# Kernel optimization log

Measured on AMD Instinct MI355X. Metric: run time of the kernel, lower is better.

The kernel has to match this reference:

```python
import jax, jax.numpy as jnp
import numpy as np

DIM = 2048
N_HEADS = 16
N_KV_HEADS = 4
HEAD_DIM = DIM // N_HEADS  # 128
N_REP = N_HEADS // N_KV_HEADS
MAX_SEQ_LEN = 4096
SEQLEN = 4096


def setup_inputs() -> dict:
    key = jax.random.key(0)
    ks = jax.random.split(key, 6)
    x = jax.random.normal(ks[0], (1, SEQLEN, DIM), dtype=jnp.float32)
    # rotary frequencies, llama-style theta=10000
    inv_freq = 1.0 / (10000.0 ** (np.arange(0, HEAD_DIM, 2, dtype=np.float32) / HEAD_DIM))
    t = np.arange(SEQLEN, dtype=np.float32)
    ang = np.outer(t, inv_freq)  # [S, head_dim/2]
    freqs_cos = jnp.asarray(np.cos(ang))
    freqs_sin = jnp.asarray(np.sin(ang))
    # additive causal mask [S, S]
    mask = jnp.where(jnp.tril(jnp.ones((SEQLEN, SEQLEN), dtype=bool)), 0.0, -1e9).astype(jnp.float32)
    sc = 0.02
    wq = jax.random.normal(ks[1], (DIM, N_HEADS * HEAD_DIM), dtype=jnp.float32) * sc
    wk = jax.random.normal(ks[2], (DIM, N_KV_HEADS * HEAD_DIM), dtype=jnp.float32) * sc
    wv = jax.random.normal(ks[3], (DIM, N_KV_HEADS * HEAD_DIM), dtype=jnp.float32) * sc
    wo = jax.random.normal(ks[4], (N_HEADS * HEAD_DIM, DIM), dtype=jnp.float32) * sc
    return {"x": x, "start_pos": 0, "freqs_cos": freqs_cos, "freqs_sin": freqs_sin,
            "mask": mask, "wq": wq, "wk": wk, "wv": wv, "wo": wo}


def _rope(x, cos, sin):
    # x: [b, s, h, d]; cos/sin: [s, d/2]; consecutive pairs form complex numbers
    b, s, h, d = x.shape
    xr = x.astype(jnp.float32).reshape(b, s, h, d // 2, 2)
    x1, x2 = xr[..., 0], xr[..., 1]
    c = cos[None, :, None, :]
    sn = sin[None, :, None, :]
    o1 = x1 * c - x2 * sn
    o2 = x1 * sn + x2 * c
    return jnp.stack([o1, o2], axis=-1).reshape(b, s, h, d).astype(x.dtype)


def reference(x, start_pos, freqs_cos, freqs_sin, mask, wq, wk, wv, wo):
    bsz, seqlen, _ = x.shape
    xq = (x @ wq).reshape(bsz, seqlen, N_HEADS, HEAD_DIM)
    xk = (x @ wk).reshape(bsz, seqlen, N_KV_HEADS, HEAD_DIM)
    xv = (x @ wv).reshape(bsz, seqlen, N_KV_HEADS, HEAD_DIM)
    xq = _rope(xq, freqs_cos, freqs_sin)
    xk = _rope(xk, freqs_cos, freqs_sin)
    # KV-cache append (cache is zeros before this call)
    cache_k = jnp.zeros((1, MAX_SEQ_LEN, N_KV_HEADS, HEAD_DIM), dtype=xk.dtype)
    cache_v = jnp.zeros((1, MAX_SEQ_LEN, N_KV_HEADS, HEAD_DIM), dtype=xv.dtype)
    cache_k = jax.lax.dynamic_update_slice(cache_k, xk, (0, start_pos, 0, 0))
    cache_v = jax.lax.dynamic_update_slice(cache_v, xv, (0, start_pos, 0, 0))
    keys = cache_k[:bsz, : start_pos + seqlen]    # [b, T, kvh, d]
    values = cache_v[:bsz, : start_pos + seqlen]
    # GQA repeat to full head count
    keys = jnp.repeat(keys, N_REP, axis=2)
    values = jnp.repeat(values, N_REP, axis=2)
    scale = 1.0 / jnp.sqrt(jnp.float32(HEAD_DIM))
    scores = jnp.einsum('bshd,bthd->bhst', xq, keys) * scale  # [b, h, s, T]
    scores = scores + mask[None, None, :, :]
    probs = jax.nn.softmax(scores.astype(jnp.float32), axis=-1).astype(xq.dtype)
    out = jnp.einsum('bhst,bthd->bshd', probs, values).reshape(bsz, seqlen, -1)
    return out @ wo
```

## Files before the change

### kernel.cpp

```cpp
#include <hip/hip_runtime.h>
#include <hip/hip_bf16.h>
#include <stdint.h>

#define SEQ 4096
#define DIM 2048
#define NH 16
#define NKV 4
#define HD 128
#define KVLD 1024


using frag8 = __attribute__((ext_vector_type(8))) short;
using f32x4 = __attribute__((ext_vector_type(4))) float;

union VecU { ushort u[8]; uint4 v; };

__device__ __forceinline__ float bf2f(ushort u) {
    union { uint32_t u; float f; } v; v.u = ((uint32_t)u) << 16; return v.f;
}
__device__ __forceinline__ ushort f2bf(float f) {
    union { float f; uint32_t u; } v; v.f = f;
    uint32_t r = v.u + 0x7fffu + ((v.u >> 16) & 1u);
    return (ushort)(r >> 16);
}

__device__ __forceinline__ void glds16(const void* g, void* l) {
    __builtin_amdgcn_global_load_lds(
        (const __attribute__((address_space(1))) void*)g,
        (__attribute__((address_space(3))) void*)l, 16, 0, 0);
}

__global__ __launch_bounds__(256) void cvt_kernel(
    const float* __restrict__ src, ushort* __restrict__ dst)
{
    size_t i = ((size_t)blockIdx.x * 256 + threadIdx.x) * 8;
    float4 f0 = *(const float4*)&src[i];
    float4 f1 = *(const float4*)&src[i + 4];
    VecU t;
    t.u[0] = f2bf(f0.x); t.u[1] = f2bf(f0.y); t.u[2] = f2bf(f0.z); t.u[3] = f2bf(f0.w);
    t.u[4] = f2bf(f1.x); t.u[5] = f2bf(f1.y); t.u[6] = f2bf(f1.z); t.u[7] = f2bf(f1.w);
    *(uint4*)&dst[i] = t.v;
}

__global__ __launch_bounds__(256) void convW_kernel(
    const float* __restrict__ wq, const float* __restrict__ wk,
    const float* __restrict__ wv, ushort* __restrict__ WqT,
    ushort* __restrict__ KVT)
{
    __shared__ ushort T[32][36];
    const int K = DIM;
    const float* src; ushort* dst; int N, bn;
    int bx = blockIdx.x;
    if (bx < 64)      { src = wq; dst = WqT;                     N = DIM; bn = bx * 32; }
    else if (bx < 80) { src = wk; dst = KVT;                     N = 512; bn = (bx - 64) * 32; }
    else              { src = wv; dst = KVT + (size_t)512 * DIM; N = 512; bn = (bx - 80) * 32; }

    int r  = threadIdx.x >> 3;
    int c4 = (threadIdx.x & 7) * 4;
    int bk = blockIdx.y * 32;
    float4 v = *(const float4*)&src[(size_t)(bk + r) * N + bn + c4];
    T[r][c4]     = f2bf(v.x); T[r][c4 + 1] = f2bf(v.y);
    T[r][c4 + 2] = f2bf(v.z); T[r][c4 + 3] = f2bf(v.w);
    __syncthreads();
    ushort4 o;
    o.x = T[c4][r]; o.y = T[c4 + 1][r]; o.z = T[c4 + 2][r]; o.w = T[c4 + 3][r];
    *(ushort4*)&dst[(size_t)(bn + r) * K + bk + c4] = o;
}

__global__ __launch_bounds__(256) void convT_kernel(
    const float* __restrict__ src, ushort* __restrict__ dst, int K, int N)
{
    __shared__ ushort T[32][36];
    int r  = threadIdx.x >> 3;
    int c4 = (threadIdx.x & 7) * 4;
    int bk = blockIdx.y * 32, bn = blockIdx.x * 32;
    float4 v = *(const float4*)&src[(size_t)(bk + r) * N + bn + c4];
    T[r][c4]     = f2bf(v.x); T[r][c4 + 1] = f2bf(v.y);
    T[r][c4 + 2] = f2bf(v.z); T[r][c4 + 3] = f2bf(v.w);
    __syncthreads();
    ushort4 o;
    o.x = T[c4][r]; o.y = T[c4 + 1][r]; o.z = T[c4 + 2][r]; o.w = T[c4 + 3][r];
    *(ushort4*)&dst[(size_t)(bn + r) * K + bk + c4] = o;
}

__global__ __launch_bounds__(256) void fuse3_kernel(
    ushort* __restrict__ Qb, ushort* __restrict__ KVb, ushort* __restrict__ VT,
    const float* __restrict__ Cos, const float* __restrict__ Sin)
{
    __shared__ ushort T[32][36];
    int b = blockIdx.x;
    if (b < 20480) {
        ushort* X; int log2nh, strideT, idx; float osc;
        if (b < 16384) { X = Qb;  log2nh = 4; strideT = DIM;  osc = 0.08838834764831845f; idx = b * 256 + threadIdx.x; }
        else           { X = KVb; log2nh = 2; strideT = KVLD; osc = 1.0f; idx = (b - 16384) * 256 + threadIdx.x; }
        int p = idx & 63;
        int h = (idx >> 6) & ((1 << log2nh) - 1);
        int t = idx >> (6 + log2nh);
        size_t base = (size_t)t * strideT + (size_t)h * 128 + 2 * p;
        ushort2 xv = *(ushort2*)&X[base];
        float x1 = bf2f(xv.x), x2 = bf2f(xv.y);
        float c = Cos[t * 64 + p], s = Sin[t * 64 + p];
        ushort2 ov;
        ov.x = f2bf((x1 * c - x2 * s) * osc);
        ov.y = f2bf((x1 * s + x2 * c) * osc);
        *(ushort2*)&X[base] = ov;
    } else {
        int v  = b - 20480;
        int bd = (v & 15) * 32;
        int bt = (v >> 4) * 32;
        int r  = threadIdx.x >> 3;
        int c4 = (threadIdx.x & 7) * 4;
        ushort4 w = *(const ushort4*)&KVb[(size_t)(bt + r) * KVLD + 512 + bd + c4];
        T[r][c4] = w.x; T[r][c4 + 1] = w.y; T[r][c4 + 2] = w.z; T[r][c4 + 3] = w.w;
        __syncthreads();
        ushort4 o;
        o.x = T[c4][r]; o.y = T[c4 + 1][r]; o.z = T[c4 + 2][r]; o.w = T[c4 + 3][r];
        *(ushort4*)&VT[(size_t)(bd + r) * SEQ + bt + c4] = o;
    }
}

template <int CF>
__global__ __launch_bounds__(256) void gemm_tn(
    const ushort* __restrict__ A, const ushort* __restrict__ BT,
    void* __restrict__ C, int M, int N, int K)
{
    __shared__ ushort As[128 * 32];
    __shared__ ushort Bs[128 * 32];

    const int tid  = threadIdx.x;
    const int lane = tid & 63;
    const int wave = tid >> 6;
    const int bm   = blockIdx.y * 128;
    const int bn   = blockIdx.x * 128;
    const int wm   = (wave >> 1) * 64;
    const int wn   = (wave & 1) * 64;
    const int quad = lane >> 4;
    const int t16  = lane & 15;
    const int kg   = quad ^ ((t16 >> 1) & 3);

    f32x4 acc[4][4] = {};

    for (int k0 = 0; k0 < K; k0 += 32) {
        #pragma unroll
        for (int it = 0; it < 2; ++it) {
            int gid = it * 256 + tid;
            int r   = gid >> 2;
            int cs  = (gid & 3) ^ ((gid >> 3) & 3);
            glds16(&A[(size_t)(bm + r) * K + k0 + cs * 8],
                   &As[(it * 256 + wave * 64) * 8]);
            glds16(&BT[(size_t)(bn + r) * K + k0 + cs * 8],
                   &Bs[(it * 256 + wave * 64) * 8]);
        }
        __syncthreads();

        frag8 af[4], bf[4];
        #pragma unroll
        for (int i = 0; i < 4; ++i)
            af[i] = *(const frag8*)&As[(wm + i * 16 + t16) * 32 + kg * 8];
        #pragma unroll
        for (int j = 0; j < 4; ++j)
            bf[j] = *(const frag8*)&Bs[(wn + j * 16 + t16) * 32 + kg * 8];
        #pragma unroll
        for (int i = 0; i < 4; ++i)
            #pragma unroll
            for (int j = 0; j < 4; ++j)
                acc[i][j] = __builtin_amdgcn_mfma_f32_16x16x32_bf16(
                    af[i], bf[j], acc[i][j], 0, 0, 0);
        __syncthreads();
    }

    #pragma unroll
    for (int i = 0; i < 4; ++i)
        #pragma unroll
        for (int j = 0; j < 4; ++j)
            #pragma unroll
            for (int r = 0; r < 4; ++r) {
                int row = bm + wm + i * 16 + quad * 4 + r;
                int col = bn + wn + j * 16 + t16;
                if (CF) ((float*)C)[(size_t)row * N + col] = acc[i][j][r];
                else    ((ushort*)C)[(size_t)row * N + col] = f2bf(acc[i][j][r]);
            }
}

__global__ __launch_bounds__(256) void gemm_qkv(
    const ushort* __restrict__ A, const ushort* __restrict__ BT,
    ushort* __restrict__ Cq, ushort* __restrict__ Ckv)
{
    const int K = DIM;
    __shared__ ushort As[128 * 32];
    __shared__ ushort Bs[128 * 32];

    const int tid  = threadIdx.x;
    const int lane = tid & 63;
    const int wave = tid >> 6;
    const int bm   = blockIdx.y * 128;
    const int bn   = blockIdx.x * 128;
    const int wm   = (wave >> 1) * 64;
    const int wn   = (wave & 1) * 64;
    const int quad = lane >> 4;
    const int t16  = lane & 15;
    const int kg   = quad ^ ((t16 >> 1) & 3);

    f32x4 acc[4][4] = {};

    for (int k0 = 0; k0 < K; k0 += 32) {
        #pragma unroll
        for (int it = 0; it < 2; ++it) {
            int gid = it * 256 + tid;
            int r   = gid >> 2;
            int cs  = (gid & 3) ^ ((gid >> 3) & 3);
            glds16(&A[(size_t)(bm + r) * K + k0 + cs * 8],
                   &As[(it * 256 + wave * 64) * 8]);
            glds16(&BT[(size_t)(bn + r) * K + k0 + cs * 8],
                   &Bs[(it * 256 + wave * 64) * 8]);
        }
        __syncthreads();

        frag8 af[4], bf[4];
        #pragma unroll
        for (int i = 0; i < 4; ++i)
            af[i] = *(const frag8*)&As[(wm + i * 16 + t16) * 32 + kg * 8];
        #pragma unroll
        for (int j = 0; j < 4; ++j)
            bf[j] = *(const frag8*)&Bs[(wn + j * 16 + t16) * 32 + kg * 8];
        #pragma unroll
        for (int i = 0; i < 4; ++i)
            #pragma unroll
            for (int j = 0; j < 4; ++j)
                acc[i][j] = __builtin_amdgcn_mfma_f32_16x16x32_bf16(
                    af[i], bf[j], acc[i][j], 0, 0, 0);
        __syncthreads();
    }

    ushort* C;
    int ldc, cb;
    if (bn < 2048) { C = Cq;  ldc = DIM;  cb = 0; }
    else           { C = Ckv; ldc = KVLD; cb = 2048; }

    #pragma unroll
    for (int i = 0; i < 4; ++i)
        #pragma unroll
        for (int j = 0; j < 4; ++j)
            #pragma unroll
            for (int r = 0; r < 4; ++r) {
                int row = bm + wm + i * 16 + quad * 4 + r;
                int col = bn + wn + j * 16 + t16;
                C[(size_t)row * ldc + (col - cb)] = f2bf(acc[i][j][r]);
            }
}

__global__ __launch_bounds__(256, 2) void attn_kernel(
    const ushort* __restrict__ Q, const ushort* __restrict__ Kb,
    const ushort* __restrict__ VT, ushort* __restrict__ Oab,
    ushort* __restrict__ Oev, float2* __restrict__ lmE, float2* __restrict__ lmO)
{
    __shared__ ushort Ks[64][136];
    __shared__ ushort Vt[128][72];
    __shared__ ushort Sp[4][32][72];

    const int tid  = threadIdx.x;
    const int lane = tid & 63;
    const int wave = tid >> 6;
    const int quad = lane >> 4;
    const int t16  = lane & 15;
    const int hp   = blockIdx.x;
    const int hA   = 2 * hp;
    const int hB   = 2 * hp + 1;
    const int kvh  = hp >> 1;

    frag8 vONE;
    #pragma unroll
    for (int i = 0; i < 8; ++i) vONE[i] = (short)0x3F80;

    const int by = (int)blockIdx.y;
    int qt, c, split;
    if (by < 64) { split = 1; qt = 63 - (by >> 1); c = by & 1; }
    else         { split = 0; qt = 95 - by;        c = 0;      }
    const int n  = qt + 1;
    const int q0 = qt * 64;
    const int qwave = q0 + wave * 16;
    const int qmaxw = qwave + 15;
    const int tstart = (split && c) ? (n / 2) * 64 : 0;
    const int tend   = (split && !c) ? (n / 2) * 64 : n * 64;

    frag8 aQA[4], aQB[4];
    #pragma unroll
    for (int kk = 0; kk < 4; ++kk) {
        aQA[kk] = *(const frag8*)&Q[(size_t)(qwave + t16) * DIM + hA * HD + kk * 32 + quad * 8];
        aQB[kk] = *(const frag8*)&Q[(size_t)(qwave + t16) * DIM + hB * HD + kk * 32 + quad * 8];
    }

    f32x4 oA[8] = {}, oB[8] = {};
    f32x4 o9A = {0.f, 0.f, 0.f, 0.f};
    f32x4 o9B = {0.f, 0.f, 0.f, 0.f};
    float mA[4] = {0.f, 0.f, 0.f, 0.f};
    float mB[4] = {0.f, 0.f, 0.f, 0.f};

    for (int t0 = tstart; t0 < tend; t0 += 64) {
        #pragma unroll
        for (int it = 0; it < 4; ++it) {
            int idx = tid + it * 256;
            int tt  = idx >> 4;
            int cc  = (idx & 15) * 8;
            *(uint4*)&Ks[tt][cc] =
                *(const uint4*)&Kb[(size_t)(t0 + tt) * KVLD + kvh * HD + cc];
        }
        #pragma unroll
        for (int it = 0; it < 4; ++it) {
            int idx = tid + it * 256;
            int d   = idx >> 3;
            int tq  = (idx & 7) * 8;
            *(uint4*)&Vt[d][tq] =
                *(const uint4*)&VT[(size_t)(kvh * HD + d) * SEQ + t0 + tq];
        }
        __syncthreads();

        const bool hi = (t0 + 32 <= qmaxw);

        f32x4 sA0 = {0.f,0.f,0.f,0.f}, sA1 = {0.f,0.f,0.f,0.f};
        f32x4 sA2 = {0.f,0.f,0.f,0.f}, sA3 = {0.f,0.f,0.f,0.f};
        f32x4 sB0 = {0.f,0.f,0.f,0.f}, sB1 = {0.f,0.f,0.f,0.f};
        f32x4 sB2 = {0.f,0.f,0.f,0.f}, sB3 = {0.f,0.f,0.f,0.f};

        __builtin_amdgcn_s_setprio(1);
        #pragma unroll
        for (int kk = 0; kk < 4; ++kk) {
            frag8 b0 = *(const frag8*)&Ks[2 * t16][kk * 32 + quad * 8];
            frag8 b1 = *(const frag8*)&Ks[2 * t16 + 1][kk * 32 + quad * 8];
            sA0 = __builtin_amdgcn_mfma_f32_16x16x32_bf16(aQA[kk], b0, sA0, 0, 0, 0);
            sB0 = __builtin_amdgcn_mfma_f32_16x16x32_bf16(aQB[kk], b0, sB0, 0, 0, 0);
            sA1 = __builtin_amdgcn_mfma_f32_16x16x32_bf16(aQA[kk], b1, sA1, 0, 0, 0);
            sB1 = __builtin_amdgcn_mfma_f32_16x16x32_bf16(aQB[kk], b1, sB1, 0, 0, 0);
        }
        if (hi) {
            #pragma unroll
            for (int kk = 0; kk < 4; ++kk) {
                frag8 b2 = *(const frag8*)&Ks[32 + 2 * t16][kk * 32 + quad * 8];
                frag8 b3 = *(const frag8*)&Ks[33 + 2 * t16][kk * 32 + quad * 8];
                sA2 = __builtin_amdgcn_mfma_f32_16x16x32_bf16(aQA[kk], b2, sA2, 0, 0, 0);
                sB2 = __builtin_amdgcn_mfma_f32_16x16x32_bf16(aQB[kk], b2, sB2, 0, 0, 0);
                sA3 = __builtin_amdgcn_mfma_f32_16x16x32_bf16(aQA[kk], b3, sA3, 0, 0, 0);
                sB3 = __builtin_amdgcn_mfma_f32_16x16x32_bf16(aQB[kk], b3, sB3, 0, 0, 0);
            }
        }
        __builtin_amdgcn_s_setprio(0);

        const bool mLo = (t0 + 31 > qwave);
        const bool mHi = (t0 + 63 > qwave);

        bool trig = false;
        #pragma unroll
        for (int r = 0; r < 4; ++r) {
            int q = qwave + quad * 4 + r;
            bool x0 = mLo && (t0 + 2 * t16 > q);
            bool x1 = mLo && (t0 + 2 * t16 + 1 > q);
            bool x2 = mHi && (t0 + 32 + 2 * t16 > q);
            bool x3 = mHi && (t0 + 33 + 2 * t16 > q);
            float vA0 = x0 ? -30000.f : sA0[r];
            float vA1 = x1 ? -30000.f : sA1[r];
            float vA2 = (hi && !x2) ? sA2[r] : -30000.f;
            float vA3 = (hi && !x3) ? sA3[r] : -30000.f;
            float vB0 = x0 ? -30000.f : sB0[r];
            float vB1 = x1 ? -30000.f : sB1[r];
            float vB2 = (hi && !x2) ? sB2[r] : -30000.f;
            float vB3 = (hi && !x3) ? sB3[r] : -30000.f;
            float lmA = fmaxf(fmaxf(vA0, vA1), fmaxf(vA2, vA3));
            float lmB = fmaxf(fmaxf(vB0, vB1), fmaxf(vB2, vB3));
            trig |= (lmA > mA[r] + 8.f) | (lmB > mB[r] + 8.f);
            float eA0 = __expf(vA0 - mA[r]);
            float eA1 = __expf(vA1 - mA[r]);
            float eB0 = __expf(vB0 - mB[r]);
            float eB1 = __expf(vB1 - mB[r]);
            *(uint*)&Sp[wave][quad * 4 + r][2 * t16] =
                (uint)f2bf(eA0) | ((uint)f2bf(eA1) << 16);
            *(uint*)&Sp[wave][16 + quad * 4 + r][2 * t16] =
                (uint)f2bf(eB0) | ((uint)f2bf(eB1) << 16);
            if (hi) {
                float eA2 = __expf(vA2 - mA[r]);
                float eA3 = __expf(vA3 - mA[r]);
                float eB2 = __expf(vB2 - mB[r]);
                float eB3 = __expf(vB3 - mB[r]);
                *(uint*)&Sp[wave][quad * 4 + r][32 + 2 * t16] =
                    (uint)f2bf(eA2) | ((uint)f2bf(eA3) << 16);
                *(uint*)&Sp[wave][16 + quad * 4 + r][32 + 2 * t16] =
                    (uint)f2bf(eB2) | ((uint)f2bf(eB3) << 16);
            }
        }

        if (__any(trig)) {
            #pragma unroll
            for (int r = 0; r < 4; ++r) {
                int q = qwave + quad * 4 + r;
                bool x0 = mLo && (t0 + 2 * t16 > q);
                bool x1 = mLo && (t0 + 2 * t16 + 1 > q);
                bool x2 = mHi && (t0 + 32 + 2 * t16 > q);
                bool x3 = mHi && (t0 + 33 + 2 * t16 > q);
                float vA0 = x0 ? -30000.f : sA0[r];
                float vA1 = x1 ? -30000.f : sA1[r];
                float vA2 = (hi && !x2) ? sA2[r] : -30000.f;
                float vA3 = (hi && !x3) ? sA3[r] : -30000.f;
                float vB0 = x0 ? -30000.f : sB0[r];
                float vB1 = x1 ? -30000.f : sB1[r];
                float vB2 = (hi && !x2) ? sB2[r] : -30000.f;
                float vB3 = (hi && !x3) ? sB3[r] : -30000.f;
                float rmA = fmaxf(fmaxf(vA0, vA1), fmaxf(vA2, vA3));
                float rmB = fmaxf(fmaxf(vB0, vB1), fmaxf(vB2, vB3));
                rmA = fmaxf(rmA, __shfl_xor(rmA, 1));
                rmA = fmaxf(rmA, __shfl_xor(rmA, 2));
                rmA = fmaxf(rmA, __shfl_xor(rmA, 4));
                rmA = fmaxf(rmA, __shfl_xor(rmA, 8));
                rmB = fmaxf(rmB, __shfl_xor(rmB, 1));
                rmB = fmaxf(rmB, __shfl_xor(rmB, 2));
                rmB = fmaxf(rmB, __shfl_xor(rmB, 4));
                rmB = fmaxf(rmB, __shfl_xor(rmB, 8));
                float mnA = fmaxf(mA[r], rmA);
                float mnB = fmaxf(mB[r], rmB);
                float alA = __expf(mA[r] - mnA);
                float alB = __expf(mB[r] - mnB);
                #pragma unroll
                for (int j = 0; j < 8; ++j) { oA[j][r] *= alA; oB[j][r] *= alB; }
                o9A[r] *= alA; o9B[r] *= alB;
                mA[r] = mnA; mB[r] = mnB;
                float eA0 = __expf(vA0 - mnA);
                float eA1 = __expf(vA1 - mnA);
                float eB0 = __expf(vB0 - mnB);
                float eB1 = __expf(vB1 - mnB);
                *(uint*)&Sp[wave][quad * 4 + r][2 * t16] =
                    (uint)f2bf(eA0) | ((uint)f2bf(eA1) << 16);
                *(uint*)&Sp[wave][16 + quad * 4 + r][2 * t16] =
                    (uint)f2bf(eB0) | ((uint)f2bf(eB1) << 16);
                if (hi) {
                    float eA2 = __expf(vA2 - mnA);
                    float eA3 = __expf(vA3 - mnA);
                    float eB2 = __expf(vB2 - mnB);
                    float eB3 = __expf(vB3 - mnB);
                    *(uint*)&Sp[wave][quad * 4 + r][32 + 2 * t16] =
                        (uint)f2bf(eA2) | ((uint)f2bf(eA3) << 16);
                    *(uint*)&Sp[wave][16 + quad * 4 + r][32 + 2 * t16] =
                        (uint)f2bf(eB2) | ((uint)f2bf(eB3) << 16);
                }
            }
        }

        frag8 aPA0 = *(const frag8*)&Sp[wave][t16][quad * 8];
        frag8 aPB0 = *(const frag8*)&Sp[wave][16 + t16][quad * 8];
        __builtin_amdgcn_s_setprio(1);
        #pragma unroll
        for (int j = 0; j < 8; ++j) {
            frag8 bV = *(const frag8*)&Vt[j * 16 + t16][quad * 8];
            oA[j] = __builtin_amdgcn_mfma_f32_16x16x32_bf16(aPA0, bV, oA[j], 0, 0, 0);
            oB[j] = __builtin_amdgcn_mfma_f32_16x16x32_bf16(aPB0, bV, oB[j], 0, 0, 0);
        }
        o9A = __builtin_amdgcn_mfma_f32_16x16x32_bf16(aPA0, vONE, o9A, 0, 0, 0);
        o9B = __builtin_amdgcn_mfma_f32_16x16x32_bf16(aPB0, vONE, o9B, 0, 0, 0);
        if (hi) {
            frag8 aPA1 = *(const frag8*)&Sp[wave][t16][32 + quad * 8];
            frag8 aPB1 = *(const frag8*)&Sp[wave][16 + t16][32 + quad * 8];
            #pragma unroll
            for (int j = 0; j < 8; ++j) {
                frag8 bV = *(const frag8*)&Vt[j * 16 + t16][32 + quad * 8];
                oA[j] = __builtin_amdgcn_mfma_f32_16x16x32_bf16(aPA1, bV, oA[j], 0, 0, 0);
                oB[j] = __builtin_amdgcn_mfma_f32_16x16x32_bf16(aPB1, bV, oB[j], 0, 0, 0);
            }
            o9A = __builtin_amdgcn_mfma_f32_16x16x32_bf16(aPA1, vONE, o9A, 0, 0, 0);
            o9B = __builtin_amdgcn_mfma_f32_16x16x32_bf16(aPB1, vONE, o9B, 0, 0, 0);
        }
        __builtin_amdgcn_s_setprio(0);
        __syncthreads();
    }

    if (split) {
        ushort* dst = c ? Oab : Oev;
        float2* lm  = c ? lmO : lmE;
        #pragma unroll
        for (int r = 0; r < 4; ++r) {
            int row = qwave + quad * 4 + r;
            if (t16 == 0) {
                lm[(size_t)(row - 2048) * NH + hA] = make_float2(o9A[r], mA[r]);
                lm[(size_t)(row - 2048) * NH + hB] = make_float2(o9B[r], mB[r]);
            }
            #pragma unroll
            for (int j = 0; j < 8; ++j) {
                dst[(size_t)row * DIM + hA * HD + j * 16 + t16] = f2bf(oA[j][r]);
                dst[(size_t)row * DIM + hB * HD + j * 16 + t16] = f2bf(oB[j][r]);
            }
        }
    } else {
        #pragma unroll
        for (int r = 0; r < 4; ++r) {
            float invA = 1.f / fmaxf(o9A[r], 1e-20f);
            float invB = 1.f / fmaxf(o9B[r], 1e-20f);
            int row = qwave + quad * 4 + r;
            #pragma unroll
            for (int j = 0; j < 8; ++j) {
                Oab[(size_t)row * DIM + hA * HD + j * 16 + t16] = f2bf(oA[j][r] * invA);
                Oab[(size_t)row * DIM + hB * HD + j * 16 + t16] = f2bf(oB[j][r] * invB);
            }
        }
    }
}

__global__ __launch_bounds__(256) void combine_kernel(
    const ushort* __restrict__ oE, const ushort* __restrict__ oO,
    const float2* __restrict__ lmE, const float2* __restrict__ lmO,
    ushort* __restrict__ out)
{
    size_t e = (size_t)(SEQ / 2) * DIM + ((size_t)blockIdx.x * 256 + threadIdx.x) * 8;
    int row = (int)(e >> 11);
    int h   = (int)((e >> 7) & 15);
    float2 LE = lmE[(size_t)(row - 2048) * NH + h];
    float2 LO = lmO[(size_t)(row - 2048) * NH + h];
    float ms = fmaxf(LE.y, LO.y);
    float aE = __expf(LE.y - ms);
    float aO = __expf(LO.y - ms);
    float inv = 1.f / fmaxf(LE.x * aE + LO.x * aO, 1e-20f);
    aE *= inv; aO *= inv;
    VecU uE, uO, uR;
    uE.v = *(const uint4*)&oE[e];
    uO.v = *(const uint4*)&oO[e];
    #pragma unroll
    for (int j = 0; j < 8; ++j)
        uR.u[j] = f2bf(bf2f(uE.u[j]) * aE + bf2f(uO.u[j]) * aO);
    *(uint4*)&out[e] = uR.v;
}

extern "C" void kernel_launch(void* const* d_in, const int* in_sizes, int n_in,
                              void* d_out, int out_size, void* d_ws, size_t ws_size,
                              hipStream_t stream)
{
    const float* x  = (const float*)d_in[0];
    const float* fc = (const float*)d_in[2];
    const float* fs = (const float*)d_in[3];
    const float* wq = (const float*)d_in[5];
    const float* wk = (const float*)d_in[6];
    const float* wv = (const float*)d_in[7];
    const float* wo = (const float*)d_in[8];

    ushort* Qb  = (ushort*)d_ws;
    ushort* KVb = Qb + (size_t)SEQ * DIM;
    ushort* Ab  = KVb + (size_t)SEQ * KVLD;
    ushort* WqT = Ab;
    ushort* KVT = Ab + (size_t)DIM * DIM;
    ushort* WoT = KVb;

    ushort* Xb = (ushort*)d_out;
    ushort* VT = Xb + (size_t)SEQ * DIM;
    float2* lmE = (float2*)(VT + (size_t)512 * SEQ);
    float2* lmO = lmE + (size_t)(SEQ / 2) * NH;

    dim3 blk(256);

    cvt_kernel<<<(SEQ * DIM) / 2048, blk, 0, stream>>>(x, Xb);
    convW_kernel<<<dim3(96, 64), blk, 0, stream>>>(wq, wk, wv, WqT, KVT);

    gemm_qkv<<<dim3(3072 / 128, SEQ / 128), blk, 0, stream>>>(Xb, Ab, Qb, KVb);

    fuse3_kernel<<<16384 + 4096 + 2048, blk, 0, stream>>>(Qb, KVb, VT, fc, fs);

    attn_kernel<<<dim3(NH / 2, 96), blk, 0, stream>>>(
        Qb, KVb, VT, Ab, Xb, lmE, lmO);

    combine_kernel<<<(SEQ / 2) * DIM / 2048, blk, 0, stream>>>(
        Xb, Ab, lmE, lmO, Ab);

    convT_kernel<<<dim3(DIM / 32, DIM / 32), blk, 0, stream>>>(wo, WoT, DIM, DIM);
    gemm_tn<1><<<dim3(DIM / 128, SEQ / 128), blk, 0, stream>>>(Ab, WoT, d_out, SEQ, DIM, DIM);
}
```

Measured before the change: 434.6 us.

## Double-buffer K/V tiles with register prefetch and shrink KV step to 32

Attention KV loop now processes 32-key tiles instead of 64, with K and V tiles double-buffered in shared memory. The next tile is prefetched into registers during compute and written to the other LDS buffer before the barrier. This is meant to hide global-load latency behind MFMA and softmax work, and to drop the half-tile causal skip logic. The cost is twice as many loop iterations and barriers, and more register pressure from the prefetch registers.

```diff
diff --git a/kernel.cpp b/kernel.cpp
--- a/kernel.cpp
+++ b/kernel.cpp
@@ -254,9 +254,9 @@
     const ushort* __restrict__ VT, ushort* __restrict__ Oab,
     ushort* __restrict__ Oev, float2* __restrict__ lmE, float2* __restrict__ lmO)
 {
-    __shared__ ushort Ks[64][136];
-    __shared__ ushort Vt[128][72];
-    __shared__ ushort Sp[4][32][72];
+    __shared__ ushort Ks[2][32][136];
+    __shared__ ushort Vt[2][128][40];
+    __shared__ ushort Sp[4][32][40];
 
     const int tid  = threadIdx.x;
     const int lane = tid & 63;
@@ -279,7 +279,6 @@
     const int n  = qt + 1;
     const int q0 = qt * 64;
     const int qwave = q0 + wave * 16;
-    const int qmaxw = qwave + 15;
     const int tstart = (split && c) ? (n / 2) * 64 : 0;
     const int tend   = (split && !c) ? (n / 2) * 64 : n * 64;
 
@@ -296,57 +295,52 @@
     float mA[4] = {0.f, 0.f, 0.f, 0.f};
     float mB[4] = {0.f, 0.f, 0.f, 0.f};
 
-    for (int t0 = tstart; t0 < tend; t0 += 64) {
-        #pragma unroll
-        for (int it = 0; it < 4; ++it) {
-            int idx = tid + it * 256;
-            int tt  = idx >> 4;
-            int cc  = (idx & 15) * 8;
-            *(uint4*)&Ks[tt][cc] =
-                *(const uint4*)&Kb[(size_t)(t0 + tt) * KVLD + kvh * HD + cc];
-        }
-        #pragma unroll
-        for (int it = 0; it < 4; ++it) {
-            int idx = tid + it * 256;
-            int d   = idx >> 3;
-            int tq  = (idx & 7) * 8;
-            *(uint4*)&Vt[d][tq] =
-                *(const uint4*)&VT[(size_t)(kvh * HD + d) * SEQ + t0 + tq];
-        }
-        __syncthreads();
-
-        const bool hi = (t0 + 32 <= qmaxw);
+    uint4 kreg[2], vreg[2];
+    const int kt0 = (tid)       >> 4, kc0 = ((tid)       & 15) * 8;
+    const int kt1 = (tid + 256) >> 4, kc1 = ((tid + 256) & 15) * 8;
+    const int vd0 = (tid)       >> 2, vq0 = ((tid)       & 3) * 8;
+    const int vd1 = (tid + 256) >> 2, vq1 = ((tid + 256) & 3) * 8;
+
+#define LOADREGS(T0)                                                          \
+    {                                                                         \
+        kreg[0] = *(const uint4*)&Kb[(size_t)((T0) + kt0) * KVLD + kvh * HD + kc0]; \
+        kreg[1] = *(const uint4*)&Kb[(size_t)((T0) + kt1) * KVLD + kvh * HD + kc1]; \
+        vreg[0] = *(const uint4*)&VT[(size_t)(kvh * HD + vd0) * SEQ + (T0) + vq0];  \
+        vreg[1] = *(const uint4*)&VT[(size_t)(kvh * HD + vd1) * SEQ + (T0) + vq1];  \
+    }
+#define WRITELDS(B)                                                           \
+    {                                                                         \
+        *(uint4*)&Ks[B][kt0][kc0] = kreg[0];                                  \
+        *(uint4*)&Ks[B][kt1][kc1] = kreg[1];                                  \
+        *(uint4*)&Vt[B][vd0][vq0] = vreg[0];                                  \
+        *(uint4*)&Vt[B][vd1][vq1] = vreg[1];                                  \
+    }
+
+    int cur = 0;
+    LOADREGS(tstart);
+    WRITELDS(0);
+    __syncthreads();
+
+    for (int t0 = tstart; t0 < tend; t0 += 32) {
+        const bool pref = (t0 + 32 < tend);
+        if (pref) LOADREGS(t0 + 32);
 
         f32x4 sA0 = {0.f,0.f,0.f,0.f}, sA1 = {0.f,0.f,0.f,0.f};
-        f32x4 sA2 = {0.f,0.f,0.f,0.f}, sA3 = {0.f,0.f,0.f,0.f};
         f32x4 sB0 = {0.f,0.f,0.f,0.f}, sB1 = {0.f,0.f,0.f,0.f};
-        f32x4 sB2 = {0.f,0.f,0.f,0.f}, sB3 = {0.f,0.f,0.f,0.f};
 
         __builtin_amdgcn_s_setprio(1);
         #pragma unroll
         for (int kk = 0; kk < 4; ++kk) {
-            frag8 b0 = *(const frag8*)&Ks[2 * t16][kk * 32 + quad * 8];
-            frag8 b1 = *(const frag8*)&Ks[2 * t16 + 1][kk * 32 + quad * 8];
+            frag8 b0 = *(const frag8*)&Ks[cur][2 * t16][kk * 32 + quad * 8];
+            frag8 b1 = *(const frag8*)&Ks[cur][2 * t16 + 1][kk * 32 + quad * 8];
             sA0 = __builtin_amdgcn_mfma_f32_16x16x32_bf16(aQA[kk], b0, sA0, 0, 0, 0);
             sB0 = __builtin_amdgcn_mfma_f32_16x16x32_bf16(aQB[kk], b0, sB0, 0, 0, 0);
             sA1 = __builtin_amdgcn_mfma_f32_16x16x32_bf16(aQA[kk], b1, sA1, 0, 0, 0);
             sB1 = __builtin_amdgcn_mfma_f32_16x16x32_bf16(aQB[kk], b1, sB1, 0, 0, 0);
         }
-        if (hi) {
-            #pragma unroll
-            for (int kk = 0; kk < 4; ++kk) {
-                frag8 b2 = *(const frag8*)&Ks[32 + 2 * t16][kk * 32 + quad * 8];
-                frag8 b3 = *(const frag8*)&Ks[33 + 2 * t16][kk * 32 + quad * 8];
-                sA2 = __builtin_amdgcn_mfma_f32_16x16x32_bf16(aQA[kk], b2, sA2, 0, 0, 0);
-                sB2 = __builtin_amdgcn_mfma_f32_16x16x32_bf16(aQB[kk], b2, sB2, 0, 0, 0);
-                sA3 = __builtin_amdgcn_mfma_f32_16x16x32_bf16(aQA[kk], b3, sA3, 0, 0, 0);
-                sB3 = __builtin_amdgcn_mfma_f32_16x16x32_bf16(aQB[kk], b3, sB3, 0, 0, 0);
-            }
-        }
         __builtin_amdgcn_s_setprio(0);
 
         const bool mLo = (t0 + 31 > qwave);
-        const bool mHi = (t0 + 63 > qwave);
 
         bool trig = false;
         #pragma unroll
@@ -354,18 +348,12 @@
             int q = qwave + quad * 4 + r;
             bool x0 = mLo && (t0 + 2 * t16 > q);
             bool x1 = mLo && (t0 + 2 * t16 + 1 > q);
-            bool x2 = mHi && (t0 + 32 + 2 * t16 > q);
-            bool x3 = mHi && (t0 + 33 + 2 * t16 > q);
             float vA0 = x0 ? -30000.f : sA0[r];
             float vA1 = x1 ? -30000.f : sA1[r];
-            float vA2 = (hi && !x2) ? sA2[r] : -30000.f;
-            float vA3 = (hi && !x3) ? sA3[r] : -30000.f;
             float vB0 = x0 ? -30000.f : sB0[r];
             float vB1 = x1 ? -30000.f : sB1[r];
-            float vB2 = (hi && !x2) ? sB2[r] : -30000.f;
-            float vB3 = (hi && !x3) ? sB3[r] : -30000.f;
-            float lmA = fmaxf(fmaxf(vA0, vA1), fmaxf(vA2, vA3));
-            float lmB = fmaxf(fmaxf(vB0, vB1), fmaxf(vB2, vB3));
+            float lmA = fmaxf(vA0, vA1);
+            float lmB = fmaxf(vB0, vB1);
             trig |= (lmA > mA[r] + 8.f) | (lmB > mB[r] + 8.f);
             float eA0 = __expf(vA0 - mA[r]);
             float eA1 = __expf(vA1 - mA[r]);
@@ -375,16 +363,6 @@
                 (uint)f2bf(eA0) | ((uint)f2bf(eA1) << 16);
             *(uint*)&Sp[wave][16 + quad * 4 + r][2 * t16] =
                 (uint)f2bf(eB0) | ((uint)f2bf(eB1) << 16);
-            if (hi) {
-                float eA2 = __expf(vA2 - mA[r]);
-                float eA3 = __expf(vA3 - mA[r]);
-                float eB2 = __expf(vB2 - mB[r]);
-                float eB3 = __expf(vB3 - mB[r]);
-                *(uint*)&Sp[wave][quad * 4 + r][32 + 2 * t16] =
-                    (uint)f2bf(eA2) | ((uint)f2bf(eA3) << 16);
-                *(uint*)&Sp[wave][16 + quad * 4 + r][32 + 2 * t16] =
-                    (uint)f2bf(eB2) | ((uint)f2bf(eB3) << 16);
-            }
         }
 
         if (__any(trig)) {
@@ -393,18 +371,12 @@
                 int q = qwave + quad * 4 + r;
                 bool x0 = mLo && (t0 + 2 * t16 > q);
                 bool x1 = mLo && (t0 + 2 * t16 + 1 > q);
-                bool x2 = mHi && (t0 + 32 + 2 * t16 > q);
-                bool x3 = mHi && (t0 + 33 + 2 * t16 > q);
                 float vA0 = x0 ? -30000.f : sA0[r];
                 float vA1 = x1 ? -30000.f : sA1[r];
-                float vA2 = (hi && !x2) ? sA2[r] : -30000.f;
-                float vA3 = (hi && !x3) ? sA3[r] : -30000.f;
                 float vB0 = x0 ? -30000.f : sB0[r];
                 float vB1 = x1 ? -30000.f : sB1[r];
-                float vB2 = (hi && !x2) ? sB2[r] : -30000.f;
-                float vB3 = (hi && !x3) ? sB3[r] : -30000.f;
-                float rmA = fmaxf(fmaxf(vA0, vA1), fmaxf(vA2, vA3));
-                float rmB = fmaxf(fmaxf(vB0, vB1), fmaxf(vB2, vB3));
+                float rmA = fmaxf(vA0, vA1);
+                float rmB = fmaxf(vB0, vB1);
                 rmA = fmaxf(rmA, __shfl_xor(rmA, 1));
                 rmA = fmaxf(rmA, __shfl_xor(rmA, 2));
                 rmA = fmaxf(rmA, __shfl_xor(rmA, 4));
@@ -429,16 +401,6 @@
                     (uint)f2bf(eA0) | ((uint)f2bf(eA1) << 16);
                 *(uint*)&Sp[wave][16 + quad * 4 + r][2 * t16] =
                     (uint)f2bf(eB0) | ((uint)f2bf(eB1) << 16);
-                if (hi) {
-                    float eA2 = __expf(vA2 - mnA);
-                    float eA3 = __expf(vA3 - mnA);
-                    float eB2 = __expf(vB2 - mnB);
-                    float eB3 = __expf(vB3 - mnB);
-                    *(uint*)&Sp[wave][quad * 4 + r][32 + 2 * t16] =
-                        (uint)f2bf(eA2) | ((uint)f2bf(eA3) << 16);
-                    *(uint*)&Sp[wave][16 + quad * 4 + r][32 + 2 * t16] =
-                        (uint)f2bf(eB2) | ((uint)f2bf(eB3) << 16);
-                }
             }
         }
 
@@ -447,27 +409,20 @@
         __builtin_amdgcn_s_setprio(1);
         #pragma unroll
         for (int j = 0; j < 8; ++j) {
-            frag8 bV = *(const frag8*)&Vt[j * 16 + t16][quad * 8];
+            frag8 bV = *(const frag8*)&Vt[cur][j * 16 + t16][quad * 8];
             oA[j] = __builtin_amdgcn_mfma_f32_16x16x32_bf16(aPA0, bV, oA[j], 0, 0, 0);
             oB[j] = __builtin_amdgcn_mfma_f32_16x16x32_bf16(aPB0, bV, oB[j], 0, 0, 0);
         }
         o9A = __builtin_amdgcn_mfma_f32_16x16x32_bf16(aPA0, vONE, o9A, 0, 0, 0);
         o9B = __builtin_amdgcn_mfma_f32_16x16x32_bf16(aPB0, vONE, o9B, 0, 0, 0);
-        if (hi) {
-            frag8 aPA1 = *(const frag8*)&Sp[wave][t16][32 + quad * 8];
-            frag8 aPB1 = *(const frag8*)&Sp[wave][16 + t16][32 + quad * 8];
-            #pragma unroll
-            for (int j = 0; j < 8; ++j) {
-                frag8 bV = *(const frag8*)&Vt[j * 16 + t16][32 + quad * 8];
-                oA[j] = __builtin_amdgcn_mfma_f32_16x16x32_bf16(aPA1, bV, oA[j], 0, 0, 0);
-                oB[j] = __builtin_amdgcn_mfma_f32_16x16x32_bf16(aPB1, bV, oB[j], 0, 0, 0);
-            }
-            o9A = __builtin_amdgcn_mfma_f32_16x16x32_bf16(aPA1, vONE, o9A, 0, 0, 0);
-            o9B = __builtin_amdgcn_mfma_f32_16x16x32_bf16(aPB1, vONE, o9B, 0, 0, 0);
-        }
         __builtin_amdgcn_s_setprio(0);
+
+        if (pref) WRITELDS(cur ^ 1);
         __syncthreads();
-    }
+        cur ^= 1;
+    }
+#undef LOADREGS
+#undef WRITELDS
 
     if (split) {
         ushort* dst = c ? Oab : Oev;
```

Measured after the change: 515.0 us. +18.5%, slower.
